# Performance work log

Hardware: AMD Instinct MI355X
Metric: run time of the kernel (lower is better)

Reference implementation:

```python
import jax, jax.numpy as jnp
import numpy as np

BLOCK = 64  # quantization block size along in_features
IN, OUT, RANK, ALPHA = 4096, 4096, 16, 32
SCALING = ALPHA / RANK


def setup_inputs() -> dict:
    key = jax.random.key(0)
    ks = jax.random.split(key, 6)
    x = jax.random.normal(ks[0], (8, 1024, IN), dtype=jnp.float32)
    # int4 codes in [0, 15]; dequant subtracts 8 -> [-8, 7]
    qweight = jax.random.randint(ks[1], (OUT, IN), 0, 16, dtype=jnp.int32)
    # blockwise absmax-style scales, small positive
    scales = jax.random.uniform(ks[2], (OUT, IN // BLOCK), dtype=jnp.float32) * 0.02 + 1e-3
    bias = jax.random.normal(ks[3], (OUT,), dtype=jnp.float32) * 0.02
    lora_A = jax.random.normal(ks[4], (IN, RANK), dtype=jnp.float32) * 0.02
    lora_B = jnp.zeros((RANK, OUT), dtype=jnp.float32)
    return {"x": x, "qweight": qweight, "scales": scales, "bias": bias,
            "lora_A": lora_A, "lora_B": lora_B}


def _dequant(qweight, scales):
    # qweight: [out, in] int codes in [0,15]; scales: [out, in/BLOCK]
    out, in_f = qweight.shape
    q = (qweight.astype(jnp.float32) - 8.0).reshape(out, in_f // BLOCK, BLOCK)
    return (q * scales[:, :, None]).reshape(out, in_f)  # [out, in]


def reference(x, qweight, scales, bias, lora_A, lora_B):
    W = _dequant(qweight, scales)                      # [out, in]
    base = jnp.einsum('bsi,oi->bso', x, W) + bias      # quantized linear
    lora = jnp.einsum('bsr,ro->bso', jnp.einsum('bsi,ir->bsr', x, lora_A), lora_B)
    return base + lora * SCALING
```

## Files before the change

### kernel.cpp

```cpp
#include <hip/hip_runtime.h>
#include <hip/hip_bf16.h>

#define IN_F 4096
#define OUT_F 4096
#define M_TOK 8192
#define RANK 16

#define CONV_BLOCKS (M_TOK * IN_F / (8 * 256))
#define DEQ_BLOCKS  2048

typedef __attribute__((ext_vector_type(16))) float f32x16;
typedef __attribute__((ext_vector_type(8))) short short8;

struct alignas(16) bf16x8_s { __hip_bfloat16 v[8]; };

__global__ __launch_bounds__(256) void prep_kernel(
    const float* __restrict__ x,
    const int* __restrict__ q,
    const float* __restrict__ scales,
    const float* __restrict__ lA,
    const float* __restrict__ lB,
    __hip_bfloat16* __restrict__ xb,
    __hip_bfloat16* __restrict__ W) {
    const int tid = threadIdx.x;

    if (blockIdx.x < CONV_BLOCKS) {
        size_t base = ((size_t)blockIdx.x * 256 + tid) * 8;
        float4 v0 = *(const float4*)(x + base);
        float4 v1 = *(const float4*)(x + base + 4);
        bf16x8_s r;
        r.v[0] = __float2bfloat16(v0.x);
        r.v[1] = __float2bfloat16(v0.y);
        r.v[2] = __float2bfloat16(v0.z);
        r.v[3] = __float2bfloat16(v0.w);
        r.v[4] = __float2bfloat16(v1.x);
        r.v[5] = __float2bfloat16(v1.y);
        r.v[6] = __float2bfloat16(v1.z);
        r.v[7] = __float2bfloat16(v1.w);
        *(bf16x8_s*)(xb + base) = r;
        return;
    }

    const int bid = blockIdx.x - CONV_BLOCKS;
    const int o0 = (bid >> 1) * 4;
    const int i0 = (bid & 1) * 2048 + tid * 8;

    float bw[16][4];
#pragma unroll
    for (int r = 0; r < 16; ++r)
#pragma unroll
        for (int oi = 0; oi < 4; ++oi)
            bw[r][oi] = 2.0f * lB[(size_t)r * OUT_F + o0 + oi];

    float fold[4][8];
#pragma unroll
    for (int e = 0; e < 8; ++e) {
        const float* ar = lA + (size_t)(i0 + e) * RANK;
        float4 a0 = *(const float4*)(ar + 0);
        float4 a1 = *(const float4*)(ar + 4);
        float4 a2 = *(const float4*)(ar + 8);
        float4 a3 = *(const float4*)(ar + 12);
#pragma unroll
        for (int oi = 0; oi < 4; ++oi) {
            float f = a0.x * bw[0][oi] + a0.y * bw[1][oi]
                    + a0.z * bw[2][oi] + a0.w * bw[3][oi]
                    + a1.x * bw[4][oi] + a1.y * bw[5][oi]
                    + a1.z * bw[6][oi] + a1.w * bw[7][oi]
                    + a2.x * bw[8][oi] + a2.y * bw[9][oi]
                    + a2.z * bw[10][oi] + a2.w * bw[11][oi]
                    + a3.x * bw[12][oi] + a3.y * bw[13][oi]
                    + a3.z * bw[14][oi] + a3.w * bw[15][oi];
            fold[oi][e] = f;
        }
    }

#pragma unroll
    for (int oi = 0; oi < 4; ++oi) {
        const int o = o0 + oi;
        const float s = scales[o * 64 + (i0 >> 6)];
        const int4* qp = (const int4*)(q + (size_t)o * IN_F + i0);
        int4 q0 = qp[0];
        int4 q1 = qp[1];
        bf16x8_s r;
        r.v[0] = __float2bfloat16(s * (float)(q0.x - 8) + fold[oi][0]);
        r.v[1] = __float2bfloat16(s * (float)(q0.y - 8) + fold[oi][1]);
        r.v[2] = __float2bfloat16(s * (float)(q0.z - 8) + fold[oi][2]);
        r.v[3] = __float2bfloat16(s * (float)(q0.w - 8) + fold[oi][3]);
        r.v[4] = __float2bfloat16(s * (float)(q1.x - 8) + fold[oi][4]);
        r.v[5] = __float2bfloat16(s * (float)(q1.y - 8) + fold[oi][5]);
        r.v[6] = __float2bfloat16(s * (float)(q1.z - 8) + fold[oi][6]);
        r.v[7] = __float2bfloat16(s * (float)(q1.w - 8) + fold[oi][7]);
        *(bf16x8_s*)(W + (size_t)o * IN_F + i0) = r;
    }
}

__global__ __launch_bounds__(256) void qlora_gemm_kernel(
    const __hip_bfloat16* __restrict__ xb,
    const __hip_bfloat16* __restrict__ Wq,
    const float* __restrict__ bias,
    float* __restrict__ out) {
    __shared__ __hip_bfloat16 As[128 * 64];
    __shared__ __hip_bfloat16 Bs[128 * 64];

    const int tid  = threadIdx.x;
    const int wave = tid >> 6;
    const int lane = tid & 63;
    const int wm = wave >> 1;
    const int wn = wave & 1;
    const int m0 = blockIdx.y * 128;
    const int n0 = blockIdx.x * 128;

    f32x16 acc[2][2];
#pragma unroll
    for (int i = 0; i < 2; ++i)
#pragma unroll
        for (int j = 0; j < 2; ++j)
#pragma unroll
            for (int e = 0; e < 16; ++e) acc[i][j][e] = 0.f;

    const int sr = lane >> 3;
    const int sc = ((lane & 7) ^ sr) * 8;

    const int frow = lane & 31;
    const int fsel = lane >> 5;

    for (int k0 = 0; k0 < IN_F; k0 += 64) {
#pragma unroll
        for (int i = 0; i < 4; ++i) {
            int c = i * 4 + wave;
            const __hip_bfloat16* ag =
                xb + (size_t)(m0 + c * 8 + sr) * IN_F + k0 + sc;
            const __hip_bfloat16* bg =
                Wq + (size_t)(n0 + c * 8 + sr) * IN_F + k0 + sc;
            __builtin_amdgcn_global_load_lds(
                (const __attribute__((address_space(1))) void*)ag,
                (__attribute__((address_space(3))) void*)(As + c * 512), 16, 0, 0);
            __builtin_amdgcn_global_load_lds(
                (const __attribute__((address_space(1))) void*)bg,
                (__attribute__((address_space(3))) void*)(Bs + c * 512), 16, 0, 0);
        }
        __syncthreads();

        const short* Asp = (const short*)As;
        const short* Bsp = (const short*)Bs;
#pragma unroll
        for (int ks = 0; ks < 4; ++ks) {
            const int g = ks * 2 + fsel;
            short8 af[2], bfv[2];
#pragma unroll
            for (int t = 0; t < 2; ++t) {
                const int arow = wm * 64 + t * 32 + frow;
                const int brow = wn * 64 + t * 32 + frow;
                af[t]  = *(const short8*)(Asp + arow * 64 + ((g ^ (arow & 7)) * 8));
                bfv[t] = *(const short8*)(Bsp + brow * 64 + ((g ^ (brow & 7)) * 8));
            }
#pragma unroll
            for (int i = 0; i < 2; ++i)
#pragma unroll
                for (int j = 0; j < 2; ++j)
                    acc[i][j] = __builtin_amdgcn_mfma_f32_32x32x16_bf16(
                        af[i], bfv[j], acc[i][j], 0, 0, 0);
        }
        __syncthreads();
    }

    const int lcol = lane & 31;
    const int rbase = 4 * (lane >> 5);
#pragma unroll
    for (int nt = 0; nt < 2; ++nt) {
        const int n = n0 + wn * 64 + nt * 32 + lcol;
        const float bv = bias[n];
#pragma unroll
        for (int mt = 0; mt < 2; ++mt) {
#pragma unroll
            for (int reg = 0; reg < 16; ++reg) {
                const int row = (reg & 3) + 8 * (reg >> 2) + rbase;
                const int m = m0 + wm * 64 + mt * 32 + row;
                out[(size_t)m * OUT_F + n] = acc[mt][nt][reg] + bv;
            }
        }
    }
}

extern "C" void kernel_launch(void* const* d_in, const int* in_sizes, int n_in,
                              void* d_out, int out_size, void* d_ws, size_t ws_size,
                              hipStream_t stream) {
    const float* x      = (const float*)d_in[0];
    const int*   qw     = (const int*)  d_in[1];
    const float* scales = (const float*)d_in[2];
    const float* bias   = (const float*)d_in[3];
    const float* lA     = (const float*)d_in[4];
    const float* lB     = (const float*)d_in[5];
    float* out = (float*)d_out;

    char* ws = (char*)d_ws;
    __hip_bfloat16* Wq = (__hip_bfloat16*)ws;
    __hip_bfloat16* xb = (__hip_bfloat16*)(ws + (size_t)32 * 1024 * 1024);

    prep_kernel<<<CONV_BLOCKS + DEQ_BLOCKS, 256, 0, stream>>>(
        x, qw, scales, lA, lB, xb, Wq);
    dim3 grid(OUT_F / 128, M_TOK / 128);
    qlora_gemm_kernel<<<grid, 256, 0, stream>>>(xb, Wq, bias, out);
}
```

Baseline: 641.8 us.

## Rewrite GEMM as 256x256 tiled, double-buffered, 8-wave ping-pong MFMA pipeline

Replaces the 128x128 single-buffered bf16 GEMM with a 256x256 tile per 512-thread block, using double-buffered LDS, staged global_load_lds prefetch interleaved across four compute phases, and 16x16x32 MFMAs with setprio scheduling. The block index is remapped so neighbouring blocks share input tiles in L2. The goal is to hide global-load latency behind MFMA work and raise arithmetic intensity per byte loaded. The cost is higher register pressure, a larger LDS footprint (128KB per block) and more fragile hand-written waitcnt and barrier logic.

```diff
diff --git a/kernel.cpp b/kernel.cpp
--- a/kernel.cpp
+++ b/kernel.cpp
@@ -9,7 +9,7 @@
 #define CONV_BLOCKS (M_TOK * IN_F / (8 * 256))
 #define DEQ_BLOCKS  2048
 
-typedef __attribute__((ext_vector_type(16))) float f32x16;
+typedef __attribute__((ext_vector_type(4))) float f32x4;
 typedef __attribute__((ext_vector_type(8))) short short8;
 
 struct alignas(16) bf16x8_s { __hip_bfloat16 v[8]; };
@@ -94,92 +94,149 @@
     }
 }
 
-__global__ __launch_bounds__(256) void qlora_gemm_kernel(
+#define BK 64
+#define NT (IN_F / BK)
+
+__device__ __forceinline__ short8 ldfrag(const short* p, int half, int row, int gran) {
+    return *(const short8*)(p + half * 8192 + row * 64 + ((gran ^ (row & 7)) * 8));
+}
+
+#define STAGE(LDSbuf, SRC, ROW0, K0)                                          \
+    {                                                                         \
+        _Pragma("unroll")                                                     \
+        for (int j = 0; j < 2; ++j) {                                         \
+            const __hip_bfloat16* g = (SRC) +                                 \
+                (size_t)((ROW0) + j * 64 + wave * 8 + srow) * IN_F + (K0) + sgc; \
+            __builtin_amdgcn_global_load_lds(                                 \
+                (const __attribute__((address_space(1))) void*)g,             \
+                (__attribute__((address_space(3))) void*)((LDSbuf) + (j * 64 + wave * 8) * 64), \
+                16, 0, 0);                                                    \
+        }                                                                     \
+    }
+
+#define PHASE(ABUF, BBUF, MH, NH, READA, STAGE_CODE, WAITCODE)                \
+    {                                                                         \
+        if (READA) {                                                          \
+            _Pragma("unroll") for (int f = 0; f < 4; ++f)                     \
+            _Pragma("unroll") for (int kk = 0; kk < 2; ++kk)                  \
+                fa[f][kk] = ldfrag(ABUF, MH, wm * 64 + f * 16 + fr, kk * 4 + fc); \
+        }                                                                     \
+        _Pragma("unroll") for (int f = 0; f < 2; ++f)                         \
+        _Pragma("unroll") for (int kk = 0; kk < 2; ++kk)                      \
+            fb[f][kk] = ldfrag(BBUF, NH, wn * 32 + f * 16 + fr, kk * 4 + fc); \
+        STAGE_CODE;                                                           \
+        WAITCODE;                                                             \
+        __builtin_amdgcn_s_barrier();                                         \
+        asm volatile("s_waitcnt lgkmcnt(0)" ::: "memory");                    \
+        __builtin_amdgcn_sched_barrier(0);                                    \
+        __builtin_amdgcn_s_setprio(1);                                        \
+        _Pragma("unroll") for (int f = 0; f < 4; ++f)                         \
+        _Pragma("unroll") for (int g2 = 0; g2 < 2; ++g2)                      \
+        _Pragma("unroll") for (int kk = 0; kk < 2; ++kk)                      \
+            acc[(MH) * 4 + f][(NH) * 2 + g2] =                                \
+                __builtin_amdgcn_mfma_f32_16x16x32_bf16(                      \
+                    fa[f][kk], fb[g2][kk], acc[(MH) * 4 + f][(NH) * 2 + g2], 0, 0, 0); \
+        __builtin_amdgcn_s_setprio(0);                                        \
+        __builtin_amdgcn_s_barrier();                                         \
+    }
+
+__global__ __launch_bounds__(512, 2) void qlora_gemm_kernel(
     const __hip_bfloat16* __restrict__ xb,
     const __hip_bfloat16* __restrict__ Wq,
     const float* __restrict__ bias,
     float* __restrict__ out) {
-    __shared__ __hip_bfloat16 As[128 * 64];
-    __shared__ __hip_bfloat16 Bs[128 * 64];
+    __shared__ __hip_bfloat16 As[2][16384];
+    __shared__ __hip_bfloat16 Bs[2][16384];
 
     const int tid  = threadIdx.x;
     const int wave = tid >> 6;
     const int lane = tid & 63;
-    const int wm = wave >> 1;
-    const int wn = wave & 1;
-    const int m0 = blockIdx.y * 128;
-    const int n0 = blockIdx.x * 128;
-
-    f32x16 acc[2][2];
-#pragma unroll
-    for (int i = 0; i < 2; ++i)
-#pragma unroll
-        for (int j = 0; j < 2; ++j)
-#pragma unroll
-            for (int e = 0; e < 16; ++e) acc[i][j][e] = 0.f;
-
-    const int sr = lane >> 3;
-    const int sc = ((lane & 7) ^ sr) * 8;
-
-    const int frow = lane & 31;
-    const int fsel = lane >> 5;
-
-    for (int k0 = 0; k0 < IN_F; k0 += 64) {
-#pragma unroll
-        for (int i = 0; i < 4; ++i) {
-            int c = i * 4 + wave;
-            const __hip_bfloat16* ag =
-                xb + (size_t)(m0 + c * 8 + sr) * IN_F + k0 + sc;
-            const __hip_bfloat16* bg =
-                Wq + (size_t)(n0 + c * 8 + sr) * IN_F + k0 + sc;
-            __builtin_amdgcn_global_load_lds(
-                (const __attribute__((address_space(1))) void*)ag,
-                (__attribute__((address_space(3))) void*)(As + c * 512), 16, 0, 0);
-            __builtin_amdgcn_global_load_lds(
-                (const __attribute__((address_space(1))) void*)bg,
-                (__attribute__((address_space(3))) void*)(Bs + c * 512), 16, 0, 0);
+    const int wm = wave >> 2;
+    const int wn = wave & 3;
+
+    const int wg = ((int)blockIdx.x & 7) * 64 + ((int)blockIdx.x >> 3);
+    const int bx = wg & 15;
+    const int by = wg >> 4;
+    const int m0 = by * 256;
+    const int n0 = bx * 256;
+
+    f32x4 acc[8][4];
+#pragma unroll
+    for (int i = 0; i < 8; ++i)
+#pragma unroll
+        for (int j = 0; j < 4; ++j)
+            acc[i][j] = (f32x4){0.f, 0.f, 0.f, 0.f};
+
+    const int srow = lane >> 3;
+    const int sgc  = ((lane & 7) ^ srow) * 8;
+
+    const int fr = lane & 15;
+    const int fc = lane >> 4;
+
+    const short* A0p = (const short*)As[0];
+    const short* A1p = (const short*)As[1];
+    const short* B0p = (const short*)Bs[0];
+    const short* B1p = (const short*)Bs[1];
+
+    short8 fa[4][2];
+    short8 fb[2][2];
+
+    STAGE(As[0],        xb, m0,       0);
+    STAGE(Bs[0],        Wq, n0,       0);
+    STAGE(As[0] + 8192, xb, m0 + 128, 0);
+    STAGE(Bs[0] + 8192, Wq, n0 + 128, 0);
+    STAGE(As[1],        xb, m0,       BK);
+    STAGE(Bs[1],        Wq, n0,       BK);
+    asm volatile("s_waitcnt vmcnt(4)" ::: "memory");
+    __builtin_amdgcn_s_barrier();
+
+    for (int it = 0; it < NT / 2; ++it) {
+        const int t = it * 2;
+        const int k_t1 = ((t + 1) & (NT - 1)) * BK;
+        const int k_t2 = ((t + 2) & (NT - 1)) * BK;
+        const int k_t3 = ((t + 3) & (NT - 1)) * BK;
+
+        PHASE(A0p, B0p, 0, 0, 1, STAGE(As[1] + 8192, xb, m0 + 128, k_t1), );
+        PHASE(A0p, B0p, 0, 1, 0, STAGE(Bs[1] + 8192, Wq, n0 + 128, k_t1), );
+        PHASE(A0p, B0p, 1, 0, 1, STAGE(As[0],        xb, m0,       k_t2), );
+        PHASE(A0p, B0p, 1, 1, 0, STAGE(Bs[0],        Wq, n0,       k_t2),
+              asm volatile("s_waitcnt vmcnt(4)" ::: "memory"));
+
+        PHASE(A1p, B1p, 0, 0, 1, STAGE(As[0] + 8192, xb, m0 + 128, k_t2), );
+        PHASE(A1p, B1p, 0, 1, 0, STAGE(Bs[0] + 8192, Wq, n0 + 128, k_t2), );
+        PHASE(A1p, B1p, 1, 0, 1, STAGE(As[1],        xb, m0,       k_t3), );
+        PHASE(A1p, B1p, 1, 1, 0, STAGE(Bs[1],        Wq, n0,       k_t3),
+              asm volatile("s_waitcnt vmcnt(4)" ::: "memory"));
+    }
+
+    asm volatile("s_waitcnt vmcnt(0)" ::: "memory");
+
+    const int cc  = lane & 15;
+    const int rr4 = (lane >> 4) * 4;
+    float bv[2][2];
+#pragma unroll
+    for (int nh = 0; nh < 2; ++nh)
+#pragma unroll
+        for (int fn = 0; fn < 2; ++fn)
+            bv[nh][fn] = bias[n0 + nh * 128 + wn * 32 + fn * 16 + cc];
+
+#pragma unroll
+    for (int mh = 0; mh < 2; ++mh)
+#pragma unroll
+        for (int fm = 0; fm < 4; ++fm) {
+            const int m = m0 + mh * 128 + wm * 64 + fm * 16 + rr4;
+#pragma unroll
+            for (int nh = 0; nh < 2; ++nh)
+#pragma unroll
+                for (int fn = 0; fn < 2; ++fn) {
+                    const int n = n0 + nh * 128 + wn * 32 + fn * 16 + cc;
+                    float* op = out + (size_t)m * OUT_F + n;
+                    const f32x4 a = acc[mh * 4 + fm][nh * 2 + fn];
+#pragma unroll
+                    for (int r = 0; r < 4; ++r)
+                        op[(size_t)r * OUT_F] = a[r] + bv[nh][fn];
+                }
         }
-        __syncthreads();
-
-        const short* Asp = (const short*)As;
-        const short* Bsp = (const short*)Bs;
-#pragma unroll
-        for (int ks = 0; ks < 4; ++ks) {
-            const int g = ks * 2 + fsel;
-            short8 af[2], bfv[2];
-#pragma unroll
-            for (int t = 0; t < 2; ++t) {
-                const int arow = wm * 64 + t * 32 + frow;
-                const int brow = wn * 64 + t * 32 + frow;
-                af[t]  = *(const short8*)(Asp + arow * 64 + ((g ^ (arow & 7)) * 8));
-                bfv[t] = *(const short8*)(Bsp + brow * 64 + ((g ^ (brow & 7)) * 8));
-            }
-#pragma unroll
-            for (int i = 0; i < 2; ++i)
-#pragma unroll
-                for (int j = 0; j < 2; ++j)
-                    acc[i][j] = __builtin_amdgcn_mfma_f32_32x32x16_bf16(
-                        af[i], bfv[j], acc[i][j], 0, 0, 0);
-        }
-        __syncthreads();
-    }
-
-    const int lcol = lane & 31;
-    const int rbase = 4 * (lane >> 5);
-#pragma unroll
-    for (int nt = 0; nt < 2; ++nt) {
-        const int n = n0 + wn * 64 + nt * 32 + lcol;
-        const float bv = bias[n];
-#pragma unroll
-        for (int mt = 0; mt < 2; ++mt) {
-#pragma unroll
-            for (int reg = 0; reg < 16; ++reg) {
-                const int row = (reg & 3) + 8 * (reg >> 2) + rbase;
-                const int m = m0 + wm * 64 + mt * 32 + row;
-                out[(size_t)m * OUT_F + n] = acc[mt][nt][reg] + bv;
-            }
-        }
-    }
 }
 
 extern "C" void kernel_launch(void* const* d_in, const int* in_sizes, int n_in,
@@ -199,6 +256,5 @@
 
     prep_kernel<<<CONV_BLOCKS + DEQ_BLOCKS, 256, 0, stream>>>(
         x, qw, scales, lA, lB, xb, Wq);
-    dim3 grid(OUT_F / 128, M_TOK / 128);
-    qlora_gemm_kernel<<<grid, 256, 0, stream>>>(xb, Wq, bias, out);
-}
+    qlora_gemm_kernel<<<dim3(512), dim3(512), 0, stream>>>(xb, Wq, bias, out);
+}
```

Result: faster. 618.6 us (-3.6%).
